# Performance work log

Measured on AMD Instinct MI355X. Metric: run time of the kernel, lower is better.

The kernel has to match this reference:

```python
import jax, jax.numpy as jnp
import numpy as np

B, N, D = 32, 512, 256   # sets, nodes-per-set, feature dim
NUM = 4                  # badmm iterations
EPS = 1e-8


def setup_inputs() -> dict:
    key = jax.random.key(0)
    ks = jax.random.split(key, 6)
    x = jax.random.normal(ks[0], (B * N, D), dtype=jnp.float32)
    # equal-size sets: to_dense_batch(x, batch) == reshape(B, N, D), mask = all ones
    batch = jnp.repeat(jnp.arange(B, dtype=jnp.int32), N)
    # learned (num,)-shaped parameters (rho/a0..a3 = None branch: 0.1*randn(num))
    a0_p = 0.1 * jax.random.normal(ks[1], (NUM,), dtype=jnp.float32)
    a1_p = 0.1 * jax.random.normal(ks[2], (NUM,), dtype=jnp.float32)
    a2_p = 0.1 * jax.random.normal(ks[3], (NUM,), dtype=jnp.float32)
    a3_p = 0.1 * jax.random.normal(ks[4], (NUM,), dtype=jnp.float32)
    rho_p = 0.1 * jax.random.normal(ks[5], (NUM,), dtype=jnp.float32)
    return {"x": x, "a0_p": a0_p, "a1_p": a1_p, "a2_p": a2_p,
            "a3_p": a3_p, "rho_p": rho_p, "batch": batch}


def _badmm_e(xd, c1, c2, p0, q0, a0, a1, a2, a3, rho, mask):
    """Log-domain Bregman ADMM for the regularized OT pooling problem
    (f_method='badmm-e').  T (B,N,D) is the transport between N samples and
    D feature slots; S is the ADMM auxiliary copy; mu/eta are the relaxed
    row/column marginals with KL priors q0/p0; z,z1,z2 are scaled duals."""
    log_p0 = jnp.log(p0 + EPS)            # (B,1,D)
    log_q0 = jnp.log(q0 + EPS)            # (B,N,1)
    log_t = log_q0 + log_p0               # (B,N,D)
    log_s = log_t
    log_mu = log_q0                       # (B,N,1) row marginal
    log_eta = log_p0                      # (B,1,D) column marginal
    z = jnp.zeros_like(log_t)
    z1 = jnp.zeros_like(log_q0)
    z2 = jnp.zeros_like(log_p0)
    neg = jnp.where(mask > 0, 0.0, -1e9)  # (B,N,1) bias masking padded rows
    for k in range(NUM):
        # T-update: rows of T sum to mu -> softmax over feature dim (axis=2)
        gw = a1[k] * jnp.einsum('bnm,bmd,bde->bne', c2, jnp.exp(log_s), c1)
        y = (xd + gw + z + rho[k] * log_s) / (rho[k] + a0[k])
        log_t = log_mu + jax.nn.log_softmax(y, axis=2)
        # S-update: columns of S sum to eta -> softmax over sample dim (axis=1)
        gw2 = a1[k] * jnp.einsum('bnm,bmd,bde->bne', c2, jnp.exp(log_t), c1)
        y2 = (gw2 - z + rho[k] * log_t) / rho[k] + neg
        log_s = log_eta + jax.nn.log_softmax(y2, axis=1)
        # marginal prox updates (KL to priors q0/p0)
        log_t1 = jax.scipy.special.logsumexp(log_t, axis=2, keepdims=True)        # (B,N,1)
        log_mu = (a2[k] * log_q0 + rho[k] * log_t1 - z1) / (a2[k] + rho[k])
        log_s1 = jax.scipy.special.logsumexp(log_s + neg, axis=1, keepdims=True)  # (B,1,D)
        log_eta = (a3[k] * log_p0 + rho[k] * log_s1 - z2) / (a3[k] + rho[k])
        # dual ascent
        z = z + rho[k] * (jnp.exp(log_t) - jnp.exp(log_s))
        z1 = z1 + rho[k] * (jnp.exp(log_mu) - jnp.exp(log_t1))
        z2 = z2 + rho[k] * (jnp.exp(log_eta) - jnp.exp(log_s1))
    return jnp.exp(log_t)


def reference(x, a0_p, a1_p, a2_p, a3_p, rho_p, batch):
    # batch = repeat(arange(B), N): equal-size sets, to_dense_batch == reshape
    xd = x.reshape(B, N, D)
    mask = jnp.ones((B, N, 1), dtype=x.dtype)
    q0 = mask / N                              # fixed q0: segment-softmax of zeros
    p0 = jnp.ones((B, 1, D), dtype=x.dtype) / D
    c1 = jnp.einsum('bnd,bne->bde', xd, xd) / N   # (B,D,D), x^T x / N
    c2 = jnp.einsum('bnd,bmd->bnm', xd, xd) / D   # (B,N,N), x x^T / D
    c1 = c1 / jnp.max(c1)
    c2 = c2 / jnp.max(c2)
    sp = jax.nn.softplus
    trans = _badmm_e(xd, c1, c2, p0, q0, sp(a0_p), sp(a1_p), sp(a2_p),
                     sp(a3_p), sp(rho_p), mask)
    frot = D * xd * trans * mask               # (B,N,D)
    return jnp.sum(frot, axis=1)               # (B,D)
```

## Files before the change

kernel.cpp:

```cpp
#include <hip/hip_runtime.h>
#include <math.h>

#define BATCH 32
#define NN 512
#define DD 256
#define NUMK 4

typedef __attribute__((ext_vector_type(8))) short bf16x8;
typedef __attribute__((ext_vector_type(4))) float f32x4;
typedef __attribute__((ext_vector_type(4))) unsigned short u16x4;

__device__ __forceinline__ float softplusf(float v) { return log1pf(expf(v)); }

__device__ __forceinline__ unsigned enc_key(float v) {
  unsigned u = __float_as_uint(v);
  return (u & 0x80000000u) ? ~u : (u | 0x80000000u);
}
__device__ __forceinline__ float dec_key(unsigned k) {
  return (k & 0x80000000u) ? __uint_as_float(k & 0x7fffffffu) : __uint_as_float(~k);
}
__device__ __forceinline__ unsigned short f2b(float f) {
  unsigned u = __float_as_uint(f);
  unsigned r = (u + 0x7fffu + ((u >> 16) & 1u)) >> 16;
  return (unsigned short)r;
}
__device__ __forceinline__ float b2f(unsigned short h) {
  return __uint_as_float(((unsigned)h) << 16);
}

#define GLDS(gp, lp)                                                   \
  __builtin_amdgcn_global_load_lds(                                    \
      (__attribute__((address_space(1))) void*)(void*)(gp),            \
      (__attribute__((address_space(3))) void*)(lp), 16, 0, 0)

__global__ __launch_bounds__(256) void k_prep(const float* __restrict__ x,
                                              short* __restrict__ xb,
                                              short* __restrict__ xTb,
                                              unsigned* keys) {
  __shared__ float t[64][65];
  int b = blockIdx.z, n0 = blockIdx.y * 64, d0 = blockIdx.x * 64;
  if (blockIdx.x == 0 && blockIdx.y == 0 && blockIdx.z == 0 && threadIdx.x == 0) {
    keys[0] = 0u; keys[1] = 0u;
  }
  const float* X = x + (size_t)b * NN * DD;
  int col = threadIdx.x & 63, rr = threadIdx.x >> 6;
#pragma unroll
  for (int s = 0; s < 16; ++s) {
    int row = s * 4 + rr;
    float v = X[(size_t)(n0 + row) * DD + d0 + col];
    t[row][col] = v;
    xb[(size_t)b * NN * DD + (size_t)(n0 + row) * DD + d0 + col] = (short)f2b(v);
  }
  __syncthreads();
#pragma unroll
  for (int s = 0; s < 16; ++s) {
    int row = s * 4 + rr;
    xTb[(size_t)b * DD * NN + (size_t)(d0 + row) * NN + n0 + col] = (short)f2b(t[col][row]);
  }
}

__global__ __launch_bounds__(256) void k_c1(const short* __restrict__ xTb,
                                            short* __restrict__ c1b,
                                            unsigned* maxslot) {
  __shared__ short As[64 * 64];
  __shared__ short Bs[64 * 64];
  const int b = blockIdx.x;
  const int m0 = blockIdx.y * 64, n0 = blockIdx.z * 64;
  const int tid = threadIdx.x, wave = tid >> 6, lane = tid & 63;
  const int ln = lane & 15, kg = lane >> 4;
  const int wr = (wave >> 1) * 32, wc = (wave & 1) * 32;
  const short* Ab = xTb + (size_t)b * ((size_t)NN * DD);

  f32x4 acc[2][2];
#pragma unroll
  for (int i = 0; i < 2; ++i)
#pragma unroll
    for (int j = 0; j < 2; ++j) acc[i][j] = (f32x4){0.f, 0.f, 0.f, 0.f};

  for (int k0 = 0; k0 < NN; k0 += 64) {
    __syncthreads();
#pragma unroll
    for (int p = 0; p < 2; ++p) {
      int row = p * 32 + wave * 8 + (lane >> 3);
      int sg = (lane & 7) ^ (row & 7);
      GLDS(Ab + (size_t)(m0 + row) * NN + k0 + sg * 8, &As[(p * 32 + wave * 8) * 64]);
      GLDS(Ab + (size_t)(n0 + row) * NN + k0 + sg * 8, &Bs[(p * 32 + wave * 8) * 64]);
    }
    __syncthreads();
    bf16x8 af[2][2], bfr[2][2];
#pragma unroll
    for (int i = 0; i < 2; ++i)
#pragma unroll
      for (int kk = 0; kk < 2; ++kk) {
        int rowA = wr + i * 16 + ln;
        af[i][kk] = *(const bf16x8*)&As[rowA * 64 + (((kk * 4 + kg) ^ (rowA & 7)) * 8)];
        int rowB = wc + i * 16 + ln;
        bfr[i][kk] = *(const bf16x8*)&Bs[rowB * 64 + (((kk * 4 + kg) ^ (rowB & 7)) * 8)];
      }
#pragma unroll
    for (int kk = 0; kk < 2; ++kk)
#pragma unroll
      for (int i = 0; i < 2; ++i)
#pragma unroll
        for (int j = 0; j < 2; ++j)
          acc[i][j] = __builtin_amdgcn_mfma_f32_16x16x32_bf16(af[i][kk], bfr[j][kk],
                                                              acc[i][j], 0, 0, 0);
  }

  unsigned short* ot = (unsigned short*)c1b + (size_t)b * ((size_t)DD * DD);
  float tmax = -1e30f;
#pragma unroll
  for (int i = 0; i < 2; ++i) {
    int r0 = m0 + wr + i * 16 + kg * 4;
#pragma unroll
    for (int j = 0; j < 2; ++j) {
      int c = n0 + wc + j * 16 + ln;
      u16x4 pk;
#pragma unroll
      for (int q = 0; q < 4; ++q) {
        float v = acc[i][j][q] * (1.0f / NN);
        tmax = fmaxf(tmax, v);
        pk[q] = f2b(v);
      }
      *(u16x4*)&ot[(size_t)c * DD + r0] = pk;
    }
  }
#pragma unroll
  for (int o = 32; o > 0; o >>= 1) tmax = fmaxf(tmax, __shfl_xor(tmax, o));
  __syncthreads();
  float* smf = (float*)As;
  if (lane == 0) smf[wave] = tmax;
  __syncthreads();
  if (tid == 0)
    atomicMax(maxslot, enc_key(fmaxf(fmaxf(smf[0], smf[1]), fmaxf(smf[2], smf[3]))));
}

__global__ __launch_bounds__(256) void k_rnmax(const short* __restrict__ xb,
                                               unsigned* maxslot) {
  const int wave = threadIdx.x >> 6, lane = threadIdx.x & 63;
  __shared__ float sm[4];
  float wmax = -1e30f;
#pragma unroll
  for (int rr = 0; rr < 8; ++rr) {
    size_t row = (size_t)blockIdx.x * 32 + wave * 8 + rr;
    u16x4 v = *(const u16x4*)(xb + row * DD + lane * 4);
    float s = 0.f;
#pragma unroll
    for (int q = 0; q < 4; ++q) {
      float f = b2f(v[q]);
      s += f * f;
    }
#pragma unroll
    for (int o = 32; o > 0; o >>= 1) s += __shfl_xor(s, o);
    wmax = fmaxf(wmax, s);
  }
  if (lane == 0) sm[wave] = wmax;
  __syncthreads();
  if (threadIdx.x == 0) {
    float m = fmaxf(fmaxf(sm[0], sm[1]), fmaxf(sm[2], sm[3])) * (1.0f / DD);
    atomicMax(maxslot, enc_key(m));
  }
}

__global__ __launch_bounds__(256) void k_misc(const short* __restrict__ c1b,
                                              const short* __restrict__ xb,
                                              float* __restrict__ s1,
                                              float* __restrict__ S,
                                              const float* a0p, const float* a1p,
                                              const float* a2p, const float* a3p,
                                              const float* rhop, float* P,
                                              const unsigned* keys) {
  int bid = blockIdx.x;
  int lane = threadIdx.x & 63;
  if (bid < 2048) {
    int row = bid * 4 + (threadIdx.x >> 6);
    u16x4 v = *(const u16x4*)(c1b + (size_t)row * 256 + lane * 4);
    float s = 0.f;
#pragma unroll
    for (int q = 0; q < 4; ++q) s += b2f(v[q]);
#pragma unroll
    for (int o = 32; o > 0; o >>= 1) s += __shfl_xor(s, o);
    if (lane == 0) s1[row] = s;
  } else if (bid < 2080) {
    int b = bid - 2048;
    int d = threadIdx.x;
    const short* X = xb + (size_t)b * NN * DD;
    float s = 0.f;
    for (int n = 0; n < NN; ++n) s += b2f((unsigned short)X[(size_t)n * DD + d]);
    S[(size_t)b * DD + d] = s;
  } else if (threadIdx.x == 0) {
    float M1 = dec_key(keys[0]);
    float M2 = dec_key(keys[1]);
    float lq0 = logf(1.0f / NN + 1e-8f);
    float lp0 = logf(1.0f / DD + 1e-8f);
    float mu = lq0, eta = lp0, z1 = 0.f, z2 = 0.f;
    for (int k = 0; k < NUMK; ++k) {
      float a0 = softplusf(a0p[k]), a1 = softplusf(a1p[k]);
      float a2 = softplusf(a2p[k]), a3 = softplusf(a3p[k]);
      float rho = softplusf(rhop[k]);
      P[0 + k] = a0;
      P[4 + k] = a1 / (M1 * M2);
      P[8 + k] = rho;
      P[12 + k] = mu;
      P[16 + k] = eta;
      float t1 = mu;
      mu = (a2 * lq0 + rho * t1 - z1) / (a2 + rho);
      z1 += rho * (expf(mu) - expf(t1));
      float s1v = eta;
      eta = (a3 * lp0 + rho * s1v - z2) / (a3 + rho);
      z2 += rho * (expf(eta) - expf(s1v));
    }
  }
}

template <int K, int OUTK>
__global__ __launch_bounds__(256) void k_gemm(
    const short* __restrict__ A, size_t sA, int lda,
    const short* __restrict__ Bp, size_t sB, int ldb,
    void* __restrict__ outp, size_t sO, int ldo,
    const float* __restrict__ P, int kiter) {
  __shared__ short As[64 * 64];
  __shared__ short Bs[64 * 64];
  const int b = blockIdx.x;
  const int m0 = blockIdx.y * 64, n0 = blockIdx.z * 64;
  const int tid = threadIdx.x, wave = tid >> 6, lane = tid & 63;
  const int ln = lane & 15, kg = lane >> 4;
  const int wr = (wave >> 1) * 32, wc = (wave & 1) * 32;
  const short* Ab = A + (size_t)b * sA;
  const short* Bb = Bp + (size_t)b * sB;

  f32x4 acc[2][2];
#pragma unroll
  for (int i = 0; i < 2; ++i)
#pragma unroll
    for (int j = 0; j < 2; ++j) acc[i][j] = (f32x4){0.f, 0.f, 0.f, 0.f};

  for (int k0 = 0; k0 < K; k0 += 64) {
    __syncthreads();
#pragma unroll
    for (int p = 0; p < 2; ++p) {
      int row = p * 32 + wave * 8 + (lane >> 3);
      int sg = (lane & 7) ^ (row & 7);
      GLDS(Ab + (size_t)(m0 + row) * lda + k0 + sg * 8, &As[(p * 32 + wave * 8) * 64]);
      GLDS(Bb + (size_t)(n0 + row) * ldb + k0 + sg * 8, &Bs[(p * 32 + wave * 8) * 64]);
    }
    __syncthreads();
    bf16x8 af[2][2], bfr[2][2];
#pragma unroll
    for (int i = 0; i < 2; ++i)
#pragma unroll
      for (int kk = 0; kk < 2; ++kk) {
        int rowA = wr + i * 16 + ln;
        af[i][kk] = *(const bf16x8*)&As[rowA * 64 + (((kk * 4 + kg) ^ (rowA & 7)) * 8)];
        int rowB = wc + i * 16 + ln;
        bfr[i][kk] = *(const bf16x8*)&Bs[rowB * 64 + (((kk * 4 + kg) ^ (rowB & 7)) * 8)];
      }
#pragma unroll
    for (int kk = 0; kk < 2; ++kk)
#pragma unroll
      for (int i = 0; i < 2; ++i)
#pragma unroll
        for (int j = 0; j < 2; ++j)
          acc[i][j] = __builtin_amdgcn_mfma_f32_16x16x32_bf16(af[i][kk], bfr[j][kk],
                                                              acc[i][j], 0, 0, 0);
  }

  unsigned short* ot = (unsigned short*)outp + (size_t)b * sO;
  if (OUTK >= 2) {
    float sc = P[4 + kiter] * (1.0f / DD);
#pragma unroll
    for (int i = 0; i < 2; ++i) {
      int r0 = m0 + wr + i * 16 + kg * 4;
#pragma unroll
      for (int j = 0; j < 2; ++j) {
        int c = n0 + wc + j * 16 + ln;
        u16x4 pk;
#pragma unroll
        for (int q = 0; q < 4; ++q) {
          float v = acc[i][j][q] * sc;
          if (OUTK == 3 && c == r0 + q) v += 1.0f;
          pk[q] = f2b(v);
        }
        *(u16x4*)&ot[(size_t)c * ldo + r0] = pk;
      }
    }
  } else {
#pragma unroll
    for (int i = 0; i < 2; ++i)
#pragma unroll
      for (int j = 0; j < 2; ++j) {
        int c = n0 + wc + j * 16 + ln;
#pragma unroll
        for (int q = 0; q < 4; ++q) {
          int r = m0 + wr + i * 16 + kg * 4 + q;
          ot[(size_t)r * ldo + c] = f2b(acc[i][j][q]);
        }
      }
  }
}

__global__ __launch_bounds__(512) void k_tsm0(
    const short* __restrict__ xTb, const float* __restrict__ S,
    const float* __restrict__ s1, short* __restrict__ eTT,
    const float* __restrict__ P) {
  const int b = blockIdx.x, n0 = blockIdx.y * 64;
  const int nl = threadIdx.x >> 3, ds = threadIdx.x & 7;
  const int n = n0 + nl;
  const size_t base = (size_t)b * ((size_t)NN * DD);
  float y[32];
  float dot = 0.f;
#pragma unroll
  for (int dk = 0; dk < 32; ++dk) {
    int d = dk * 8 + ds;
    float v = b2f((unsigned short)xTb[base + (size_t)d * NN + n]);
    y[dk] = v;
    dot += v * S[(size_t)b * DD + d];
  }
  dot += __shfl_xor(dot, 1);
  dot += __shfl_xor(dot, 2);
  dot += __shfl_xor(dot, 4);
  const float c0 = logf(1.0f / NN + 1e-8f) + logf(1.0f / DD + 1e-8f);
  float g = P[4] * expf(c0) * dot * (1.0f / DD);
  float inv = 1.0f / (P[8] + P[0]);
  float m = -1e30f;
#pragma unroll
  for (int dk = 0; dk < 32; ++dk) {
    int d = dk * 8 + ds;
    y[dk] = (y[dk] + g * s1[(size_t)b * DD + d]) * inv;
    m = fmaxf(m, y[dk]);
  }
  m = fmaxf(m, __shfl_xor(m, 1));
  m = fmaxf(m, __shfl_xor(m, 2));
  m = fmaxf(m, __shfl_xor(m, 4));
  float s = 0.f;
#pragma unroll
  for (int dk = 0; dk < 32; ++dk) s += expf(y[dk] - m);
  s += __shfl_xor(s, 1);
  s += __shfl_xor(s, 2);
  s += __shfl_xor(s, 4);
  const float lse = m + logf(s);
  const float mu = P[12];
#pragma unroll
  for (int dk = 0; dk < 32; ++dk) {
    int d = dk * 8 + ds;
    eTT[base + (size_t)d * NN + n] = (short)f2b(expf(mu + y[dk] - lse));
  }
}

template <int LAST>
__global__ __launch_bounds__(256) void k_ft(
    const short* __restrict__ xb, const short* __restrict__ Mtb,
    const short* __restrict__ eST, const short* __restrict__ zb,
    short* __restrict__ eTT, const short* __restrict__ xTb,
    float* __restrict__ part, const float* __restrict__ P, int kiter) {
  __shared__ short As[32 * 64];
  __shared__ short Bs[256 * 64];
  const int b = blockIdx.x, m0 = blockIdx.y * 32;
  const int tid = threadIdx.x, wave = tid >> 6, lane = tid & 63;
  const int ln = lane & 15, kg = lane >> 4;
  const short* Ab = xb + (size_t)b * ((size_t)NN * DD);
  const short* Bb = Mtb + (size_t)b * ((size_t)DD * DD);
  const size_t base = (size_t)b * ((size_t)NN * DD);

  f32x4 acc[2][4];
#pragma unroll
  for (int i = 0; i < 2; ++i)
#pragma unroll
    for (int j = 0; j < 4; ++j) acc[i][j] = (f32x4){0.f, 0.f, 0.f, 0.f};

  for (int k0 = 0; k0 < DD; k0 += 64) {
    __syncthreads();
    {
      int row = wave * 8 + (lane >> 3);
      int sg = (lane & 7) ^ (row & 7);
      GLDS(Ab + (size_t)(m0 + row) * DD + k0 + sg * 8, &As[(wave * 8) * 64]);
    }
#pragma unroll
    for (int c = 0; c < 8; ++c) {
      int row = wave * 64 + c * 8 + (lane >> 3);
      int sg = (lane & 7) ^ (row & 7);
      GLDS(Bb + (size_t)row * DD + k0 + sg * 8, &Bs[(wave * 64 + c * 8) * 64]);
    }
    __syncthreads();
    bf16x8 af[2][2], bfr[4][2];
#pragma unroll
    for (int i = 0; i < 2; ++i)
#pragma unroll
      for (int kk = 0; kk < 2; ++kk) {
        int rowA = i * 16 + ln;
        af[i][kk] = *(const bf16x8*)&As[rowA * 64 + (((kk * 4 + kg) ^ (rowA & 7)) * 8)];
      }
#pragma unroll
    for (int j = 0; j < 4; ++j)
#pragma unroll
      for (int kk = 0; kk < 2; ++kk) {
        int rowB = wave * 64 + j * 16 + ln;
        bfr[j][kk] = *(const bf16x8*)&Bs[rowB * 64 + (((kk * 4 + kg) ^ (rowB & 7)) * 8)];
      }
#pragma unroll
    for (int kk = 0; kk < 2; ++kk)
#pragma unroll
      for (int i = 0; i < 2; ++i)
#pragma unroll
        for (int j = 0; j < 4; ++j)
          acc[i][j] = __builtin_amdgcn_mfma_f32_16x16x32_bf16(af[i][kk], bfr[j][kk],
                                                              acc[i][j], 0, 0, 0);
  }
  __syncthreads();
  float* red = (float*)As;

  const float a0 = P[kiter], rho = P[8 + kiter], mu = P[12 + kiter];
  const float inv = 1.0f / (rho + a0);
  float y[2][4][4];
#pragma unroll
  for (int i = 0; i < 2; ++i)
#pragma unroll
    for (int j = 0; j < 4; ++j) {
      int d = wave * 64 + j * 16 + ln;
      int n4 = m0 + i * 16 + kg * 4;
      size_t idx = base + (size_t)d * NN + n4;
      u16x4 zv = *(const u16x4*)&zb[idx];
      u16x4 es = *(const u16x4*)&eST[idx];
#pragma unroll
      for (int q = 0; q < 4; ++q)
        y[i][j][q] = (acc[i][j][q] + b2f(zv[q]) + rho * logf(b2f(es[q]))) * inv;
    }
  float pm[2][4];
#pragma unroll
  for (int i = 0; i < 2; ++i)
#pragma unroll
    for (int q = 0; q < 4; ++q) {
      float m = fmaxf(fmaxf(y[i][0][q], y[i][1][q]), fmaxf(y[i][2][q], y[i][3][q]));
      m = fmaxf(m, __shfl_xor(m, 1));
      m = fmaxf(m, __shfl_xor(m, 2));
      m = fmaxf(m, __shfl_xor(m, 4));
      m = fmaxf(m, __shfl_xor(m, 8));
      pm[i][q] = m;
    }
  if (ln == 0) {
#pragma unroll
    for (int i = 0; i < 2; ++i)
#pragma unroll
      for (int q = 0; q < 4; ++q) red[wave * 32 + i * 16 + kg * 4 + q] = pm[i][q];
  }
  __syncthreads();
  if (tid < 32)
    red[128 + tid] = fmaxf(fmaxf(red[tid], red[32 + tid]),
                           fmaxf(red[64 + tid], red[96 + tid]));
  __syncthreads();
  float sm[2][4], mc[2][4];
#pragma unroll
  for (int i = 0; i < 2; ++i)
#pragma unroll
    for (int q = 0; q < 4; ++q) {
      mc[i][q] = red[128 + i * 16 + kg * 4 + q];
      float s = expf(y[i][0][q] - mc[i][q]) + expf(y[i][1][q] - mc[i][q]) +
                expf(y[i][2][q] - mc[i][q]) + expf(y[i][3][q] - mc[i][q]);
      s += __shfl_xor(s, 1);
      s += __shfl_xor(s, 2);
      s += __shfl_xor(s, 4);
      s += __shfl_xor(s, 8);
      sm[i][q] = s;
    }
  __syncthreads();
  if (ln == 0) {
#pragma unroll
    for (int i = 0; i < 2; ++i)
#pragma unroll
      for (int q = 0; q < 4; ++q) red[wave * 32 + i * 16 + kg * 4 + q] = sm[i][q];
  }
  __syncthreads();
  if (tid < 32)
    red[160 + tid] = red[128 + tid] +
                     logf(red[tid] + red[32 + tid] + red[64 + tid] + red[96 + tid]);
  __syncthreads();
  float lse[2][4];
#pragma unroll
  for (int i = 0; i < 2; ++i)
#pragma unroll
    for (int q = 0; q < 4; ++q) lse[i][q] = red[160 + i * 16 + kg * 4 + q];

  if (LAST == 0) {
#pragma unroll
    for (int i = 0; i < 2; ++i)
#pragma unroll
      for (int j = 0; j < 4; ++j) {
        int d = wave * 64 + j * 16 + ln;
        int n4 = m0 + i * 16 + kg * 4;
        size_t idx = base + (size_t)d * NN + n4;
        u16x4 et;
#pragma unroll
        for (int q = 0; q < 4; ++q) et[q] = f2b(expf(mu + y[i][j][q] - lse[i][q]));
        *(u16x4*)&eTT[idx] = et;
      }
  } else {
    float p[4] = {0.f, 0.f, 0.f, 0.f};
#pragma unroll
    for (int j = 0; j < 4; ++j)
#pragma unroll
      for (int i = 0; i < 2; ++i) {
        int d = wave * 64 + j * 16 + ln;
        int n4 = m0 + i * 16 + kg * 4;
        size_t idx = base + (size_t)d * NN + n4;
        u16x4 xv = *(const u16x4*)&xTb[idx];
#pragma unroll
        for (int q = 0; q < 4; ++q)
          p[j] += b2f(xv[q]) * expf(mu + y[i][j][q] - lse[i][q]);
      }
#pragma unroll
    for (int j = 0; j < 4; ++j) {
      p[j] += __shfl_xor(p[j], 16);
      p[j] += __shfl_xor(p[j], 32);
    }
    if (kg == 0) {
      size_t pb = ((size_t)b * 16 + blockIdx.y) * DD;
#pragma unroll
      for (int j = 0; j < 4; ++j) part[pb + wave * 64 + j * 16 + ln] = p[j];
    }
  }
}

template <int ZFIRST>
__global__ __launch_bounds__(512) void k_fs(
    const short* __restrict__ xb, const short* __restrict__ Mtb,
    const short* __restrict__ eTT, short* __restrict__ eST,
    short* __restrict__ zb, const float* __restrict__ P, int kiter) {
  __shared__ short As[512 * 32];
  __shared__ short Bs[32 * 32];
  const int b = blockIdx.x, m0 = blockIdx.y * 32;
  const int tid = threadIdx.x, wave = tid >> 6, lane = tid & 63;
  const int ln = lane & 15, kg = lane >> 4;
  const short* Ab = xb + (size_t)b * ((size_t)NN * DD);
  const short* Bb = Mtb + (size_t)b * ((size_t)DD * DD);
  const size_t base = (size_t)b * ((size_t)NN * DD);

  f32x4 acc[4][2];
#pragma unroll
  for (int i = 0; i < 4; ++i)
#pragma unroll
    for (int j = 0; j < 2; ++j) acc[i][j] = (f32x4){0.f, 0.f, 0.f, 0.f};

  for (int k0 = 0; k0 < DD; k0 += 32) {
    __syncthreads();
#pragma unroll
    for (int c = 0; c < 4; ++c) {
      int row = wave * 64 + c * 16 + (lane >> 2);
      int sg = (lane & 3) ^ (row & 3);
      GLDS(Ab + (size_t)row * DD + k0 + sg * 8, &As[(wave * 64 + c * 16) * 32]);
    }
    if (wave < 2) {
      int row = wave * 16 + (lane >> 2);
      int sg = (lane & 3) ^ (row & 3);
      GLDS(Bb + (size_t)(m0 + row) * DD + k0 + sg * 8, &Bs[(wave * 16) * 32]);
    }
    __syncthreads();
    bf16x8 af[4], bfr[2];
#pragma unroll
    for (int i = 0; i < 4; ++i) {
      int rowA = wave * 64 + i * 16 + ln;
      af[i] = *(const bf16x8*)&As[rowA * 32 + ((kg ^ (rowA & 3)) * 8)];
    }
#pragma unroll
    for (int j = 0; j < 2; ++j) {
      int rowB = j * 16 + ln;
      bfr[j] = *(const bf16x8*)&Bs[rowB * 32 + ((kg ^ (rowB & 3)) * 8)];
    }
#pragma unroll
    for (int i = 0; i < 4; ++i)
#pragma unroll
      for (int j = 0; j < 2; ++j)
        acc[i][j] = __builtin_amdgcn_mfma_f32_16x16x32_bf16(af[i], bfr[j], acc[i][j], 0, 0, 0);
  }
  __syncthreads();
  float* red = (float*)Bs;

  const float rho = P[8 + kiter], eta = P[16 + kiter];
  const float invr = 1.0f / rho;
  float y[4][2][4];
  u16x4 etr[4][2], zr[4][2];
#pragma unroll
  for (int i = 0; i < 4; ++i)
#pragma unroll
    for (int j = 0; j < 2; ++j) {
      int d = m0 + j * 16 + ln;
      int n4 = wave * 64 + i * 16 + kg * 4;
      size_t idx = base + (size_t)d * NN + n4;
      etr[i][j] = *(const u16x4*)&eTT[idx];
      if (!ZFIRST) zr[i][j] = *(const u16x4*)&zb[idx];
#pragma unroll
      for (int q = 0; q < 4; ++q) {
        float zf = ZFIRST ? 0.0f : b2f(zr[i][j][q]);
        y[i][j][q] = (acc[i][j][q] - zf + rho * logf(b2f(etr[i][j][q]))) * invr;
      }
    }
  float pm[2];
#pragma unroll
  for (int j = 0; j < 2; ++j) {
    float m = -1e30f;
#pragma unroll
    for (int i = 0; i < 4; ++i)
#pragma unroll
      for (int q = 0; q < 4; ++q) m = fmaxf(m, y[i][j][q]);
    m = fmaxf(m, __shfl_xor(m, 16));
    m = fmaxf(m, __shfl_xor(m, 32));
    pm[j] = m;
  }
  if (kg == 0) {
#pragma unroll
    for (int j = 0; j < 2; ++j) red[wave * 32 + j * 16 + ln] = pm[j];
  }
  __syncthreads();
  if (tid < 32) {
    float M = red[tid];
#pragma unroll
    for (int w = 1; w < 8; ++w) M = fmaxf(M, red[w * 32 + tid]);
    red[256 + tid] = M;
  }
  __syncthreads();
  float mc[2], ps[2];
#pragma unroll
  for (int j = 0; j < 2; ++j) {
    mc[j] = red[256 + j * 16 + ln];
    float s = 0.f;
#pragma unroll
    for (int i = 0; i < 4; ++i)
#pragma unroll
      for (int q = 0; q < 4; ++q) s += expf(y[i][j][q] - mc[j]);
    s += __shfl_xor(s, 16);
    s += __shfl_xor(s, 32);
    ps[j] = s;
  }
  __syncthreads();
  if (kg == 0) {
#pragma unroll
    for (int j = 0; j < 2; ++j) red[wave * 32 + j * 16 + ln] = ps[j];
  }
  __syncthreads();
  if (tid < 32) {
    float S = 0.f;
#pragma unroll
    for (int w = 0; w < 8; ++w) S += red[w * 32 + tid];
    red[288 + tid] = red[256 + tid] + logf(S);
  }
  __syncthreads();
  float lse[2];
#pragma unroll
  for (int j = 0; j < 2; ++j) lse[j] = red[288 + j * 16 + ln];

#pragma unroll
  for (int i = 0; i < 4; ++i)
#pragma unroll
    for (int j = 0; j < 2; ++j) {
      int d = m0 + j * 16 + ln;
      int n4 = wave * 64 + i * 16 + kg * 4;
      size_t idx = base + (size_t)d * NN + n4;
      u16x4 ev, zo;
#pragma unroll
      for (int q = 0; q < 4; ++q) {
        float es = expf(eta + y[i][j][q] - lse[j]);
        ev[q] = f2b(es);
        float zf = ZFIRST ? 0.0f : b2f(zr[i][j][q]);
        zo[q] = f2b(zf + rho * (b2f(etr[i][j][q]) - es));
      }
      *(u16x4*)&eST[idx] = ev;
      *(u16x4*)&zb[idx] = zo;
    }
}

__global__ __launch_bounds__(256) void k_out2(const float* __restrict__ part,
                                              float* __restrict__ out) {
  int b = blockIdx.x, d = threadIdx.x;
  float acc = 0.0f;
#pragma unroll
  for (int c = 0; c < 16; ++c) acc += part[((size_t)b * 16 + c) * DD + d];
  out[(size_t)b * DD + d] = (float)DD * acc;
}

extern "C" void kernel_launch(void* const* d_in, const int* in_sizes, int n_in,
                              void* d_out, int out_size, void* d_ws, size_t ws_size,
                              hipStream_t stream) {
  const float* x = (const float*)d_in[0];
  const float* a0p = (const float*)d_in[1];
  const float* a1p = (const float*)d_in[2];
  const float* a2p = (const float*)d_in[3];
  const float* a3p = (const float*)d_in[4];
  const float* rhop = (const float*)d_in[5];
  float* out = (float*)d_out;

  const size_t NE = (size_t)BATCH * NN * DD;
  const size_t NE_b = (size_t)NN * DD;
  const size_t C1_b = (size_t)DD * DD;

  float* fws = (float*)d_ws;
  float* S = fws;
  float* s1 = S + BATCH * DD;
  float* part = s1 + BATCH * DD;
  float* P = part + BATCH * 16 * DD;
  unsigned* keys = (unsigned*)(P + 24);
  short* sws = (short*)(keys + 8);
  short* xb = sws;
  short* xTb = sws + NE;
  short* eTT = sws + 2 * NE;
  short* eST = sws + 3 * NE;
  short* zb = sws + 4 * NE;
  short* Fb = sws + 5 * NE;
  short* Mtb = Fb + (size_t)BATCH * C1_b;
  short* c1b = Mtb + (size_t)BATCH * C1_b;

  k_prep<<<dim3(4, 8, BATCH), 256, 0, stream>>>(x, xb, xTb, keys);
  k_c1<<<dim3(BATCH, 4, 4), 256, 0, stream>>>(xTb, c1b, keys + 0);
  k_rnmax<<<512, 256, 0, stream>>>(xb, keys + 1);
  k_misc<<<2081, 256, 0, stream>>>(c1b, xb, s1, S, a0p, a1p, a2p, a3p, rhop, P, keys);

  k_tsm0<<<dim3(BATCH, 8), 512, 0, stream>>>(xTb, S, s1, eTT, P);
  k_gemm<512, 1><<<dim3(BATCH, 4, 4), 256, 0, stream>>>(
      xTb, NE_b, NN, eTT, NE_b, NN, (void*)Fb, C1_b, DD, nullptr, 0);
  k_gemm<256, 2><<<dim3(BATCH, 4, 4), 256, 0, stream>>>(
      Fb, C1_b, DD, c1b, C1_b, DD, (void*)Mtb, C1_b, DD, P, 0);
  k_fs<1><<<dim3(BATCH, 8), 512, 0, stream>>>(xb, Mtb, eTT, eST, zb, P, 0);

  for (int k = 1; k <= 2; ++k) {
    k_gemm<512, 1><<<dim3(BATCH, 4, 4), 256, 0, stream>>>(
        xTb, NE_b, NN, eST, NE_b, NN, (void*)Fb, C1_b, DD, nullptr, 0);
    k_gemm<256, 3><<<dim3(BATCH, 4, 4), 256, 0, stream>>>(
        Fb, C1_b, DD, c1b, C1_b, DD, (void*)Mtb, C1_b, DD, P, k);
    k_ft<0><<<dim3(BATCH, 16), 256, 0, stream>>>(xb, Mtb, eST, zb, eTT, xTb,
                                                 part, P, k);
    k_gemm<512, 1><<<dim3(BATCH, 4, 4), 256, 0, stream>>>(
        xTb, NE_b, NN, eTT, NE_b, NN, (void*)Fb, C1_b, DD, nullptr, 0);
    k_gemm<256, 2><<<dim3(BATCH, 4, 4), 256, 0, stream>>>(
        Fb, C1_b, DD, c1b, C1_b, DD, (void*)Mtb, C1_b, DD, P, k);
    k_fs<0><<<dim3(BATCH, 8), 512, 0, stream>>>(xb, Mtb, eTT, eST, zb, P, k);
  }

  k_gemm<512, 1><<<dim3(BATCH, 4, 4), 256, 0, stream>>>(
      xTb, NE_b, NN, eST, NE_b, NN, (void*)Fb, C1_b, DD, nullptr, 0);
  k_gemm<256, 3><<<dim3(BATCH, 4, 4), 256, 0, stream>>>(
      Fb, C1_b, DD, c1b, C1_b, DD, (void*)Mtb, C1_b, DD, P, 3);
  k_ft<1><<<dim3(BATCH, 16), 256, 0, stream>>>(xb, Mtb, eST, zb, eTT, xTb,
                                               part, P, 3);
  k_out2<<<BATCH, 256, 0, stream>>>(part, out);
}
```

Before: 241.9 us.

## Load GEMM fragments directly from global with register double-buffering; coalesce tsm0 reads

```diff
diff --git a/kernel.cpp b/kernel.cpp
--- a/kernel.cpp
+++ b/kernel.cpp
@@ -303,46 +303,54 @@
     const short* __restrict__ xTb, const float* __restrict__ S,
     const float* __restrict__ s1, short* __restrict__ eTT,
     const float* __restrict__ P) {
-  const int b = blockIdx.x, n0 = blockIdx.y * 64;
-  const int nl = threadIdx.x >> 3, ds = threadIdx.x & 7;
-  const int n = n0 + nl;
+  const int b = blockIdx.x;
+  const int n = blockIdx.y * 64 + (threadIdx.x & 63);
+  const int wave = threadIdx.x >> 6, lane = threadIdx.x & 63;
   const size_t base = (size_t)b * ((size_t)NN * DD);
+  __shared__ float red[8][64];
   float y[32];
   float dot = 0.f;
 #pragma unroll
   for (int dk = 0; dk < 32; ++dk) {
-    int d = dk * 8 + ds;
+    int d = wave * 32 + dk;
     float v = b2f((unsigned short)xTb[base + (size_t)d * NN + n]);
     y[dk] = v;
     dot += v * S[(size_t)b * DD + d];
   }
-  dot += __shfl_xor(dot, 1);
-  dot += __shfl_xor(dot, 2);
-  dot += __shfl_xor(dot, 4);
+  red[wave][lane] = dot;
+  __syncthreads();
+  dot = 0.f;
+#pragma unroll
+  for (int w = 0; w < 8; ++w) dot += red[w][lane];
   const float c0 = logf(1.0f / NN + 1e-8f) + logf(1.0f / DD + 1e-8f);
-  float g = P[4] * expf(c0) * dot * (1.0f / DD);
-  float inv = 1.0f / (P[8] + P[0]);
+  const float g = P[4] * expf(c0) * dot * (1.0f / DD);
+  const float inv = 1.0f / (P[8] + P[0]);
   float m = -1e30f;
 #pragma unroll
   for (int dk = 0; dk < 32; ++dk) {
-    int d = dk * 8 + ds;
+    int d = wave * 32 + dk;
     y[dk] = (y[dk] + g * s1[(size_t)b * DD + d]) * inv;
     m = fmaxf(m, y[dk]);
   }
-  m = fmaxf(m, __shfl_xor(m, 1));
-  m = fmaxf(m, __shfl_xor(m, 2));
-  m = fmaxf(m, __shfl_xor(m, 4));
+  __syncthreads();
+  red[wave][lane] = m;
+  __syncthreads();
+#pragma unroll
+  for (int w = 0; w < 8; ++w) m = fmaxf(m, red[w][lane]);
   float s = 0.f;
 #pragma unroll
   for (int dk = 0; dk < 32; ++dk) s += expf(y[dk] - m);
-  s += __shfl_xor(s, 1);
-  s += __shfl_xor(s, 2);
-  s += __shfl_xor(s, 4);
+  __syncthreads();
+  red[wave][lane] = s;
+  __syncthreads();
+  s = 0.f;
+#pragma unroll
+  for (int w = 0; w < 8; ++w) s += red[w][lane];
   const float lse = m + logf(s);
   const float mu = P[12];
 #pragma unroll
   for (int dk = 0; dk < 32; ++dk) {
-    int d = dk * 8 + ds;
+    int d = wave * 32 + dk;
     eTT[base + (size_t)d * NN + n] = (short)f2b(expf(mu + y[dk] - lse));
   }
 }
@@ -353,8 +361,7 @@
     const short* __restrict__ eST, const short* __restrict__ zb,
     short* __restrict__ eTT, const short* __restrict__ xTb,
     float* __restrict__ part, const float* __restrict__ P, int kiter) {
-  __shared__ short As[32 * 64];
-  __shared__ short Bs[256 * 64];
+  __shared__ float red[192];
   const int b = blockIdx.x, m0 = blockIdx.y * 32;
   const int tid = threadIdx.x, wave = tid >> 6, lane = tid & 63;
   const int ln = lane & 15, kg = lane >> 4;
@@ -362,55 +369,54 @@
   const short* Bb = Mtb + (size_t)b * ((size_t)DD * DD);
   const size_t base = (size_t)b * ((size_t)NN * DD);
 
+  const short* Ar[2];
+#pragma unroll
+  for (int i = 0; i < 2; ++i)
+    Ar[i] = Ab + (size_t)(m0 + i * 16 + ln) * DD + kg * 8;
+  const short* Br[4];
+#pragma unroll
+  for (int j = 0; j < 4; ++j)
+    Br[j] = Bb + (size_t)(wave * 64 + j * 16 + ln) * DD + kg * 8;
+
   f32x4 acc[2][4];
 #pragma unroll
   for (int i = 0; i < 2; ++i)
 #pragma unroll
     for (int j = 0; j < 4; ++j) acc[i][j] = (f32x4){0.f, 0.f, 0.f, 0.f};
 
-  for (int k0 = 0; k0 < DD; k0 += 64) {
-    __syncthreads();
-    {
-      int row = wave * 8 + (lane >> 3);
-      int sg = (lane & 7) ^ (row & 7);
-      GLDS(Ab + (size_t)(m0 + row) * DD + k0 + sg * 8, &As[(wave * 8) * 64]);
-    }
-#pragma unroll
-    for (int c = 0; c < 8; ++c) {
-      int row = wave * 64 + c * 8 + (lane >> 3);
-      int sg = (lane & 7) ^ (row & 7);
-      GLDS(Bb + (size_t)row * DD + k0 + sg * 8, &Bs[(wave * 64 + c * 8) * 64]);
-    }
-    __syncthreads();
-    bf16x8 af[2][2], bfr[4][2];
-#pragma unroll
-    for (int i = 0; i < 2; ++i)
-#pragma unroll
-      for (int kk = 0; kk < 2; ++kk) {
-        int rowA = i * 16 + ln;
-        af[i][kk] = *(const bf16x8*)&As[rowA * 64 + (((kk * 4 + kg) ^ (rowA & 7)) * 8)];
-      }
-#pragma unroll
-    for (int j = 0; j < 4; ++j)
-#pragma unroll
-      for (int kk = 0; kk < 2; ++kk) {
-        int rowB = wave * 64 + j * 16 + ln;
-        bfr[j][kk] = *(const bf16x8*)&Bs[rowB * 64 + (((kk * 4 + kg) ^ (rowB & 7)) * 8)];
-      }
-#pragma unroll
-    for (int kk = 0; kk < 2; ++kk)
+  {
+    bf16x8 a0[2], b0[4], a1[2], b1[4];
+#pragma unroll
+    for (int i = 0; i < 2; ++i) a0[i] = *(const bf16x8*)(Ar[i]);
+#pragma unroll
+    for (int j = 0; j < 4; ++j) b0[j] = *(const bf16x8*)(Br[j]);
+#pragma unroll
+    for (int k0 = 0; k0 < DD; k0 += 64) {
+#pragma unroll
+      for (int i = 0; i < 2; ++i) a1[i] = *(const bf16x8*)(Ar[i] + k0 + 32);
+#pragma unroll
+      for (int j = 0; j < 4; ++j) b1[j] = *(const bf16x8*)(Br[j] + k0 + 32);
 #pragma unroll
       for (int i = 0; i < 2; ++i)
 #pragma unroll
         for (int j = 0; j < 4; ++j)
-          acc[i][j] = __builtin_amdgcn_mfma_f32_16x16x32_bf16(af[i][kk], bfr[j][kk],
-                                                              acc[i][j], 0, 0, 0);
-  }
-  __syncthreads();
-  float* red = (float*)As;
-
-  const float a0 = P[kiter], rho = P[8 + kiter], mu = P[12 + kiter];
-  const float inv = 1.0f / (rho + a0);
+          acc[i][j] = __builtin_amdgcn_mfma_f32_16x16x32_bf16(a0[i], b0[j], acc[i][j], 0, 0, 0);
+      if (k0 + 64 < DD) {
+#pragma unroll
+        for (int i = 0; i < 2; ++i) a0[i] = *(const bf16x8*)(Ar[i] + k0 + 64);
+#pragma unroll
+        for (int j = 0; j < 4; ++j) b0[j] = *(const bf16x8*)(Br[j] + k0 + 64);
+      }
+#pragma unroll
+      for (int i = 0; i < 2; ++i)
+#pragma unroll
+        for (int j = 0; j < 4; ++j)
+          acc[i][j] = __builtin_amdgcn_mfma_f32_16x16x32_bf16(a1[i], b1[j], acc[i][j], 0, 0, 0);
+    }
+  }
+
+  const float a0p_ = P[kiter], rho = P[8 + kiter], mu = P[12 + kiter];
+  const float inv = 1.0f / (rho + a0p_);
   float y[2][4][4];
 #pragma unroll
   for (int i = 0; i < 2; ++i)
@@ -525,8 +531,7 @@
     const short* __restrict__ xb, const short* __restrict__ Mtb,
     const short* __restrict__ eTT, short* __restrict__ eST,
     short* __restrict__ zb, const float* __restrict__ P, int kiter) {
-  __shared__ short As[512 * 32];
-  __shared__ short Bs[32 * 32];
+  __shared__ float red[320];
   const int b = blockIdx.x, m0 = blockIdx.y * 32;
   const int tid = threadIdx.x, wave = tid >> 6, lane = tid & 63;
   const int ln = lane & 15, kg = lane >> 4;
@@ -534,45 +539,51 @@
   const short* Bb = Mtb + (size_t)b * ((size_t)DD * DD);
   const size_t base = (size_t)b * ((size_t)NN * DD);
 
+  const short* Ar[4];
+#pragma unroll
+  for (int i = 0; i < 4; ++i)
+    Ar[i] = Ab + (size_t)(wave * 64 + i * 16 + ln) * DD + kg * 8;
+  const short* Br[2];
+#pragma unroll
+  for (int j = 0; j < 2; ++j)
+    Br[j] = Bb + (size_t)(m0 + j * 16 + ln) * DD + kg * 8;
+
   f32x4 acc[4][2];
 #pragma unroll
   for (int i = 0; i < 4; ++i)
 #pragma unroll
     for (int j = 0; j < 2; ++j) acc[i][j] = (f32x4){0.f, 0.f, 0.f, 0.f};
 
-  for (int k0 = 0; k0 < DD; k0 += 32) {
-    __syncthreads();
-#pragma unroll
-    for (int c = 0; c < 4; ++c) {
-      int row = wave * 64 + c * 16 + (lane >> 2);
-      int sg = (lane & 3) ^ (row & 3);
-      GLDS(Ab + (size_t)row * DD + k0 + sg * 8, &As[(wave * 64 + c * 16) * 32]);
-    }
-    if (wave < 2) {
-      int row = wave * 16 + (lane >> 2);
-      int sg = (lane & 3) ^ (row & 3);
-      GLDS(Bb + (size_t)(m0 + row) * DD + k0 + sg * 8, &Bs[(wave * 16) * 32]);
-    }
-    __syncthreads();
-    bf16x8 af[4], bfr[2];
-#pragma unroll
-    for (int i = 0; i < 4; ++i) {
-      int rowA = wave * 64 + i * 16 + ln;
-      af[i] = *(const bf16x8*)&As[rowA * 32 + ((kg ^ (rowA & 3)) * 8)];
-    }
-#pragma unroll
-    for (int j = 0; j < 2; ++j) {
-      int rowB = j * 16 + ln;
-      bfr[j] = *(const bf16x8*)&Bs[rowB * 32 + ((kg ^ (rowB & 3)) * 8)];
-    }
-#pragma unroll
-    for (int i = 0; i < 4; ++i)
-#pragma unroll
-      for (int j = 0; j < 2; ++j)
-        acc[i][j] = __builtin_amdgcn_mfma_f32_16x16x32_bf16(af[i], bfr[j], acc[i][j], 0, 0, 0);
-  }
-  __syncthreads();
-  float* red = (float*)Bs;
+  {
+    bf16x8 a0[4], b0[2], a1[4], b1[2];
+#pragma unroll
+    for (int i = 0; i < 4; ++i) a0[i] = *(const bf16x8*)(Ar[i]);
+#pragma unroll
+    for (int j = 0; j < 2; ++j) b0[j] = *(const bf16x8*)(Br[j]);
+#pragma unroll
+    for (int k0 = 0; k0 < DD; k0 += 64) {
+#pragma unroll
+      for (int i = 0; i < 4; ++i) a1[i] = *(const bf16x8*)(Ar[i] + k0 + 32);
+#pragma unroll
+      for (int j = 0; j < 2; ++j) b1[j] = *(const bf16x8*)(Br[j] + k0 + 32);
+#pragma unroll
+      for (int i = 0; i < 4; ++i)
+#pragma unroll
+        for (int j = 0; j < 2; ++j)
+          acc[i][j] = __builtin_amdgcn_mfma_f32_16x16x32_bf16(a0[i], b0[j], acc[i][j], 0, 0, 0);
+      if (k0 + 64 < DD) {
+#pragma unroll
+        for (int i = 0; i < 4; ++i) a0[i] = *(const bf16x8*)(Ar[i] + k0 + 64);
+#pragma unroll
+        for (int j = 0; j < 2; ++j) b0[j] = *(const bf16x8*)(Br[j] + k0 + 64);
+      }
+#pragma unroll
+      for (int i = 0; i < 4; ++i)
+#pragma unroll
+        for (int j = 0; j < 2; ++j)
+          acc[i][j] = __builtin_amdgcn_mfma_f32_16x16x32_bf16(a1[i], b1[j], acc[i][j], 0, 0, 0);
+    }
+  }
 
   const float rho = P[8 + kiter], eta = P[16 + kiter];
   const float invr = 1.0f / rho;
```

New measurement: 266.9 us. 10.4% more time.
